# Kernel optimization log

Hardware: AMD Instinct MI355X
Metric: run time of the kernel (lower is better)

## Reference

```python
import jax, jax.numpy as jnp
import numpy as np

B, H, W, C, WS, NH, NL, ND = 64, 32, 32, 96, 8, 6, 4, 6
N = WS * WS
HD = C // NH
SC = HD ** -0.5


def _rel_pos_index():
    coords = np.stack(np.meshgrid(np.arange(WS), np.arange(WS), indexing='ij')).reshape(2, -1)
    rel = (coords[:, :, None] - coords[:, None, :]).transpose(1, 2, 0)
    rel[..., 0] += WS - 1
    rel[..., 1] += WS - 1
    rel[..., 0] *= 2 * WS - 1
    return jnp.asarray(rel.sum(-1))  # [N, N] int


def _attn_mask():
    shift = WS // 2
    img = np.zeros((H, W))
    cnt = 0
    for hs in (slice(0, -WS), slice(-WS, -shift), slice(-shift, None)):
        for ws_ in (slice(0, -WS), slice(-WS, -shift), slice(-shift, None)):
            img[hs, ws_] = cnt
            cnt += 1
    mw = img.reshape(H // WS, WS, W // WS, WS).transpose(0, 2, 1, 3).reshape(-1, N)
    am = mw[:, None, :] - mw[:, :, None]
    return jnp.asarray(np.where(am != 0, -100.0, 0.0).astype(np.float32))  # [nW, N, N]


RPI = _rel_pos_index()
AMASK = _attn_mask()


def ln(x, s, b):
    m = x.mean(-1, keepdims=True)
    v = ((x - m) ** 2).mean(-1, keepdims=True)
    return (x - m) * jax.lax.rsqrt(v + 1e-5) * s + b


def conv3(x, w, b):
    return jax.lax.conv_general_dilated(x, w, (1, 1), 'SAME', dimension_numbers=('NHWC', 'HWIO', 'NHWC')) + b


def win_part(x):  # (B,H,W,C) -> (B*nW, N, C)
    b = x.shape[0]
    return x.reshape(b, H // WS, WS, W // WS, WS, C).transpose(0, 1, 3, 2, 4, 5).reshape(-1, N, C)


def win_rev(xw, b):  # (B*nW, N, C) -> (B,H,W,C)
    return xw.reshape(b, H // WS, W // WS, WS, WS, C).transpose(0, 1, 3, 2, 4, 5).reshape(b, H, W, C)


def swin_block(x, shift, p):
    n1s, n1b, qw, qb, pw, pb, rpb, n2s, n2b, f1w, f1b, f2w, f2b = p
    b = x.shape[0]
    h = ln(x, n1s, n1b).reshape(b, H, W, C)
    if shift:
        h = jnp.roll(h, (-shift, -shift), (1, 2))
    xw = win_part(h)
    qkv = (xw @ qw + qb).reshape(-1, N, 3, NH, HD).transpose(2, 0, 3, 1, 4)
    q, k, v = qkv[0], qkv[1], qkv[2]  # each (B*nW, NH, N, HD)
    attn = (q * SC) @ k.transpose(0, 1, 3, 2)  # (B*nW, NH, N, N)
    bias = rpb[RPI.reshape(-1)].reshape(N, N, NH).transpose(2, 0, 1)
    attn = attn + bias[None]
    if shift:
        nW = AMASK.shape[0]
        attn = (attn.reshape(b, nW, NH, N, N) + AMASK[None, :, None]).reshape(-1, NH, N, N)
    attn = jax.nn.softmax(attn, -1)
    o = (attn @ v).transpose(0, 2, 1, 3).reshape(-1, N, C) @ pw + pb
    h = win_rev(o, b)
    if shift:
        h = jnp.roll(h, (shift, shift), (1, 2))
    x = x + h.reshape(b, H * W, C)
    y = ln(x, n2s, n2b)
    return x + jax.nn.gelu(y @ f1w + f1b, approximate=False) @ f2w + f2b


def setup_inputs() -> dict:
    key = jax.random.key(0)
    ks = iter(jax.random.split(key, 40))
    nrm = lambda shape: jax.random.normal(next(ks), shape, jnp.float32) * 0.02
    d = {
        'es_input': jax.random.normal(next(ks), (B, 2, H, W), jnp.float32),
        'j_plus_input': jax.random.normal(next(ks), (B, 2, H, W), jnp.float32),
        'conv_first_w': nrm((3, 3, 4, C)), 'conv_first_b': jnp.zeros((C,), jnp.float32),
        'pe_norm_s': jnp.ones((C,), jnp.float32), 'pe_norm_b': jnp.zeros((C,), jnp.float32),
        'n1_s': jnp.ones((NL, ND, C), jnp.float32), 'n1_b': jnp.zeros((NL, ND, C), jnp.float32),
        'qkv_w': nrm((NL, ND, C, 3 * C)), 'qkv_b': jnp.zeros((NL, ND, 3 * C), jnp.float32),
        'proj_w': nrm((NL, ND, C, C)), 'proj_b': jnp.zeros((NL, ND, C), jnp.float32),
        'rpb': nrm((NL, ND, (2 * WS - 1) ** 2, NH)),
        'n2_s': jnp.ones((NL, ND, C), jnp.float32), 'n2_b': jnp.zeros((NL, ND, C), jnp.float32),
        'fc1_w': nrm((NL, ND, C, 4 * C)), 'fc1_b': jnp.zeros((NL, ND, 4 * C), jnp.float32),
        'fc2_w': nrm((NL, ND, 4 * C, C)), 'fc2_b': jnp.zeros((NL, ND, C), jnp.float32),
        'rstb_conv_w': nrm((NL, 3, 3, C, C)), 'rstb_conv_b': jnp.zeros((NL, C), jnp.float32),
        'normf_s': jnp.ones((C,), jnp.float32), 'normf_b': jnp.zeros((C,), jnp.float32),
        'body_w': nrm((3, 3, C, C)), 'body_b': jnp.zeros((C,), jnp.float32),
        'last_w': nrm((3, 3, C, 2)), 'last_b': jnp.zeros((2,), jnp.float32),
    }
    return d


def reference(es_input, j_plus_input, conv_first_w, conv_first_b, pe_norm_s, pe_norm_b,
              n1_s, n1_b, qkv_w, qkv_b, proj_w, proj_b, rpb, n2_s, n2_b,
              fc1_w, fc1_b, fc2_w, fc2_b, rstb_conv_w, rstb_conv_b,
              normf_s, normf_b, body_w, body_b, last_w, last_b):
    x0 = jnp.concatenate([es_input, j_plus_input], 1).transpose(0, 2, 3, 1)  # NHWC, C=4
    xf = conv3(x0, conv_first_w, conv_first_b)  # shallow feature, [B,H,W,96]
    x = ln(xf.reshape(B, H * W, C), pe_norm_s, pe_norm_b)  # patch_embed norm
    for l in range(NL):
        r = x
        for d in range(ND):
            p = (n1_s[l, d], n1_b[l, d], qkv_w[l, d], qkv_b[l, d], proj_w[l, d], proj_b[l, d],
                 rpb[l, d], n2_s[l, d], n2_b[l, d], fc1_w[l, d], fc1_b[l, d], fc2_w[l, d], fc2_b[l, d])
            x = swin_block(x, 0 if d % 2 == 0 else WS // 2, p)
        x = conv3(x.reshape(B, H, W, C), rstb_conv_w[l], rstb_conv_b[l]).reshape(B, H * W, C) + r
    x = ln(x, normf_s, normf_b).reshape(B, H, W, C)
    res = conv3(x, body_w, body_b) + xf
    out = conv3(res, last_w, last_b)  # [B,H,W,2]
    return out.transpose(0, 3, 1, 2)
```

## Files before the change

kernel.cpp:

```cpp
#include <hip/hip_runtime.h>
#include <hip/hip_bf16.h>
#include <cstddef>
#include <cstdint>

#define BB 64
#define HH 32
#define WW_ 32
#define CC 96
#define WS 8
#define NH 6
#define NL 4
#define ND 6
#define T_TOK (BB*HH*WW_)
#define TC ((size_t)T_TOK*CC)

typedef long long ll;
typedef __attribute__((ext_vector_type(8))) short short8;
typedef __attribute__((ext_vector_type(4))) float f32x4;
typedef __attribute__((ext_vector_type(4))) unsigned short ushort4v;

__global__ void JNetSwinIR_41034117546277_kernel() {}

__device__ __forceinline__ unsigned short f2bf(float f) {
  unsigned u = __float_as_uint(f);
  unsigned r = (u + 0x7FFF + ((u >> 16) & 1)) >> 16;
  return (unsigned short)r;
}
__device__ __forceinline__ float bf2f(unsigned short h) {
  return __uint_as_float(((unsigned)h) << 16);
}

__global__ __launch_bounds__(256) void fill_kernel(float* p, float v, int n)
{
  const int idx = blockIdx.x * 256 + threadIdx.x;
  if (idx < n) p[idx] = v;
}

__global__ __launch_bounds__(256) void wconv_kernel(
    const float* __restrict__ W, unsigned short* __restrict__ Wt, int K, int N)
{
  const int ld = blockIdx.y;
  const int idx = blockIdx.x * 256 + threadIdx.x;
  if (idx >= K * N) return;
  const int k = idx / N, n = idx % N;
  Wt[(size_t)ld * K * N + (size_t)n * K + k] = f2bf(W[(size_t)ld * K * N + idx]);
}

__global__ __launch_bounds__(256) void wconv_conv_kernel(
    const float* __restrict__ W, unsigned short* __restrict__ Wt, int total)
{
  const int idx = blockIdx.x * 256 + threadIdx.x;
  if (idx >= total) return;
  const int l9 = idx / 9216;
  const int rest = idx % 9216;
  const int oc = rest / 96, ic = rest % 96;
  Wt[idx] = f2bf(W[(size_t)(l9 * 96 + ic) * 96 + oc]);
}

__global__ __launch_bounds__(256) void ln_fp32_kernel(
    const float* __restrict__ x, const float* __restrict__ gamma,
    const float* __restrict__ beta, float* __restrict__ out)
{
  const int wave = threadIdx.x >> 6;
  const int lane = threadIdx.x & 63;
  const int t = blockIdx.x * 4 + wave;
  const float* xp = x + (size_t)t * CC;
  const float v0 = xp[lane];
  const float v1 = (lane < 32) ? xp[64 + lane] : 0.f;
  float s = v0 + v1, s2 = v0 * v0 + v1 * v1;
  #pragma unroll
  for (int off = 32; off; off >>= 1) {
    s  += __shfl_xor(s,  off);
    s2 += __shfl_xor(s2, off);
  }
  const float mean = s * (1.f / 96.f);
  const float var  = s2 * (1.f / 96.f) - mean * mean;
  const float inv  = rsqrtf(var + 1e-5f);
  float* op = out + (size_t)t * CC;
  const float r0 = (v0 - mean) * inv * gamma[lane] + beta[lane];
  const float r1 = (v1 - mean) * inv * gamma[64 + lane] + beta[64 + lane];
  op[lane] = r0;
  if (lane < 32) op[64 + lane] = r1;
}

__global__ __launch_bounds__(384) void swin_block_fused(
    float* x, const float* __restrict__ n1s, const float* __restrict__ n1b,
    const unsigned short* __restrict__ wq_ld, const float* __restrict__ qkvb,
    const float* __restrict__ rpb_ld,
    const unsigned short* __restrict__ wp_ld, const float* __restrict__ projb,
    const float* __restrict__ n2s, const float* __restrict__ n2b,
    const unsigned short* __restrict__ w1_ld, const float* __restrict__ f1b,
    const unsigned short* __restrict__ w2_ld, const float* __restrict__ f2b,
    int shift)
{
  const int widx = blockIdx.x;
  const int tid  = threadIdx.x;
  const int wv   = tid >> 6;
  const int lane = tid & 63;

  __shared__ __attribute__((aligned(16))) char smem[72472];
  auto a    = (unsigned short(*)[104])(smem);
  auto kk   = (float(*)[100])(smem + 13312);
  auto xacc = (float(*)[100])(smem + 13312);
  auto vv   = (unsigned short(*)[104])(smem + 38912);
  auto hbuf = (unsigned short(*)[200])(smem + 38912);
  auto qt   = (unsigned short(*)[112])(smem + 52224);
  float* bias_s = (float*)(smem + 66560);
  int*   reg_s  = (int*)(smem + 71960);
  int*   st_s   = (int*)(smem + 72216);

  if (tid < 64) {
    const int wimg = widx & 15;
    const int h = (wimg >> 2) * 8 + (tid >> 3);
    const int w = (wimg & 3) * 8 + (tid & 7);
    reg_s[tid] = 3 * (h < 24 ? 0 : (h < 28 ? 1 : 2)) +
                     (w < 24 ? 0 : (w < 28 ? 1 : 2));
    const int b = widx >> 4;
    const int p = (h + shift) & 31, q = (w + shift) & 31;
    st_s[tid] = (b << 10) + (p << 5) + q;
  }
  for (int i = tid; i < NH * 225; i += 384) {
    const int hh = i / 225, ii = i % 225;
    bias_s[i] = rpb_ld[ii * NH + hh];
  }
  __syncthreads();

  for (int t = wv; t < 64; t += 6) {
    const float* xp = x + (size_t)st_s[t] * CC;
    const float v0 = xp[lane];
    const float v1 = (lane < 32) ? xp[64 + lane] : 0.f;
    float s = v0 + v1, s2 = v0 * v0 + v1 * v1;
    #pragma unroll
    for (int off = 32; off; off >>= 1) {
      s  += __shfl_xor(s,  off);
      s2 += __shfl_xor(s2, off);
    }
    const float mean = s * (1.f / 96.f);
    const float var  = s2 * (1.f / 96.f) - mean * mean;
    const float inv  = rsqrtf(var + 1e-5f);
    a[t][lane] = f2bf((v0 - mean) * inv * n1s[lane] + n1b[lane]);
    if (lane < 32)
      a[t][64 + lane] = f2bf((v1 - mean) * inv * n1s[64 + lane] + n1b[64 + lane]);
  }
  __syncthreads();

  {
    const int row = lane & 15;
    const int ko  = (lane >> 4) * 8;
    const int cc  = lane & 15;
    const int cr0 = (lane >> 4) * 4;
    #pragma unroll
    for (int out3 = 0; out3 < 3; ++out3) {
      const int n0 = out3 * 96 + wv * 16;
      const unsigned short* bp = wq_ld + (size_t)(n0 + row) * 96 + ko;
      const float bz = qkvb[n0 + cc];
      #pragma unroll
      for (int rt = 0; rt < 4; ++rt) {
        f32x4 acc = {0.f, 0.f, 0.f, 0.f};
        const unsigned short* ap = &a[rt * 16 + row][ko];
        #pragma unroll
        for (int k0 = 0; k0 < 96; k0 += 32) {
          const short8 af = *(const short8*)(ap + k0);
          const short8 bf = *(const short8*)(bp + k0);
          acc = __builtin_amdgcn_mfma_f32_16x16x32_bf16(af, bf, acc, 0, 0, 0);
        }
        #pragma unroll
        for (int r = 0; r < 4; ++r) {
          const int tok = rt * 16 + cr0 + r;
          const float v = acc[r] + bz;
          if (out3 == 0)      qt[tok][wv * 16 + cc] = f2bf(v);
          else if (out3 == 1) kk[tok][wv * 16 + cc] = v;
          else                vv[tok][wv * 16 + cc] = f2bf(v);
        }
      }
    }
  }
  __syncthreads();

  const int head = wv;
  {
    float q[16];
    {
      const short8 q0 = *(const short8*)&qt[lane][head * 16];
      const short8 q1 = *(const short8*)&qt[lane][head * 16 + 8];
      #pragma unroll
      for (int i = 0; i < 8; ++i) {
        q[i]     = bf2f((unsigned short)q0[i]);
        q[8 + i] = bf2f((unsigned short)q1[i]);
      }
    }
    const float* bias_h = bias_s + head * 225;
    const int ih = lane >> 3, iw = lane & 7;
    const int myreg = reg_s[lane];
    float s[64];
    #pragma unroll
    for (int j = 0; j < 64; ++j) {
      const float4 k0 = *(const float4*)&kk[j][head * 16];
      const float4 k1 = *(const float4*)&kk[j][head * 16 + 4];
      const float4 k2 = *(const float4*)&kk[j][head * 16 + 8];
      const float4 k3 = *(const float4*)&kk[j][head * 16 + 12];
      float acc = 0.f;
      acc = fmaf(q[0],  k0.x, acc); acc = fmaf(q[1],  k0.y, acc);
      acc = fmaf(q[2],  k0.z, acc); acc = fmaf(q[3],  k0.w, acc);
      acc = fmaf(q[4],  k1.x, acc); acc = fmaf(q[5],  k1.y, acc);
      acc = fmaf(q[6],  k1.z, acc); acc = fmaf(q[7],  k1.w, acc);
      acc = fmaf(q[8],  k2.x, acc); acc = fmaf(q[9],  k2.y, acc);
      acc = fmaf(q[10], k2.z, acc); acc = fmaf(q[11], k2.w, acc);
      acc = fmaf(q[12], k3.x, acc); acc = fmaf(q[13], k3.y, acc);
      acc = fmaf(q[14], k3.z, acc); acc = fmaf(q[15], k3.w, acc);
      const int idx = (ih - (j >> 3) + 7) * 15 + (iw - (j & 7) + 7);
      acc = acc * 0.25f + bias_h[idx];
      if (shift && reg_s[j] != myreg) acc -= 100.f;
      s[j] = acc;
    }
    float m = s[0];
    #pragma unroll
    for (int j = 1; j < 64; ++j) m = fmaxf(m, s[j]);
    float sum = 0.f;
    #pragma unroll
    for (int j = 0; j < 64; ++j) { const float p = __expf(s[j] - m); s[j] = p; sum += p; }
    const float inv = 1.f / sum;
    float o[16] = {};
    #pragma unroll
    for (int j = 0; j < 64; ++j) {
      const float p = s[j] * inv;
      const short8 v0 = *(const short8*)&vv[j][head * 16];
      const short8 v1 = *(const short8*)&vv[j][head * 16 + 8];
      #pragma unroll
      for (int i = 0; i < 8; ++i) {
        o[i]     = fmaf(p, bf2f((unsigned short)v0[i]), o[i]);
        o[8 + i] = fmaf(p, bf2f((unsigned short)v1[i]), o[8 + i]);
      }
    }
    short8 o0, o1;
    #pragma unroll
    for (int i = 0; i < 8; ++i) {
      o0[i] = (short)f2bf(o[i]);
      o1[i] = (short)f2bf(o[8 + i]);
    }
    *(short8*)&a[lane][head * 16]     = o0;
    *(short8*)&a[lane][head * 16 + 8] = o1;
  }
  __syncthreads();

  {
    const int row = lane & 15;
    const int ko  = (lane >> 4) * 8;
    const int cc  = lane & 15;
    const int cr0 = (lane >> 4) * 4;
    const int n0 = wv * 16;
    const unsigned short* bp = wp_ld + (size_t)(n0 + row) * 96 + ko;
    const float bz = projb[n0 + cc];
    #pragma unroll
    for (int rt = 0; rt < 4; ++rt) {
      f32x4 acc = {0.f, 0.f, 0.f, 0.f};
      const unsigned short* ap = &a[rt * 16 + row][ko];
      #pragma unroll
      for (int k0 = 0; k0 < 96; k0 += 32) {
        const short8 af = *(const short8*)(ap + k0);
        const short8 bf = *(const short8*)(bp + k0);
        acc = __builtin_amdgcn_mfma_f32_16x16x32_bf16(af, bf, acc, 0, 0, 0);
      }
      #pragma unroll
      for (int r = 0; r < 4; ++r) {
        const int tok = rt * 16 + cr0 + r;
        const float xo = x[(size_t)st_s[tok] * CC + n0 + cc];
        xacc[tok][n0 + cc] = xo + acc[r] + bz;
      }
    }
  }
  __syncthreads();

  for (int t = wv; t < 64; t += 6) {
    const float v0 = xacc[t][lane];
    const float v1 = (lane < 32) ? xacc[t][64 + lane] : 0.f;
    float s = v0 + v1, s2 = v0 * v0 + v1 * v1;
    #pragma unroll
    for (int off = 32; off; off >>= 1) {
      s  += __shfl_xor(s,  off);
      s2 += __shfl_xor(s2, off);
    }
    const float mean = s * (1.f / 96.f);
    const float var  = s2 * (1.f / 96.f) - mean * mean;
    const float inv  = rsqrtf(var + 1e-5f);
    a[t][lane] = f2bf((v0 - mean) * inv * n2s[lane] + n2b[lane]);
    if (lane < 32)
      a[t][64 + lane] = f2bf((v1 - mean) * inv * n2s[64 + lane] + n2b[64 + lane]);
  }
  __syncthreads();

  const int row = lane & 15;
  const int ko  = (lane >> 4) * 8;
  const int cc  = lane & 15;
  const int cr0 = (lane >> 4) * 4;
  f32x4 acc2[4];
  #pragma unroll
  for (int i = 0; i < 4; ++i) acc2[i] = (f32x4){0.f, 0.f, 0.f, 0.f};
  #pragma unroll
  for (int p = 0; p < 2; ++p) {
    #pragma unroll
    for (int ct = 0; ct < 2; ++ct) {
      const int n0g = p * 192 + wv * 32 + ct * 16;
      const int n0l = wv * 32 + ct * 16;
      const unsigned short* bp = w1_ld + (size_t)(n0g + row) * 96 + ko;
      const float bz = f1b[n0g + cc];
      #pragma unroll
      for (int rt = 0; rt < 4; ++rt) {
        f32x4 acc = {0.f, 0.f, 0.f, 0.f};
        const unsigned short* ap = &a[rt * 16 + row][ko];
        #pragma unroll
        for (int k0 = 0; k0 < 96; k0 += 32) {
          const short8 af = *(const short8*)(ap + k0);
          const short8 bf = *(const short8*)(bp + k0);
          acc = __builtin_amdgcn_mfma_f32_16x16x32_bf16(af, bf, acc, 0, 0, 0);
        }
        #pragma unroll
        for (int r = 0; r < 4; ++r) {
          float v = acc[r] + bz;
          v = 0.5f * v * (1.f + erff(v * 0.70710678118f));
          hbuf[rt * 16 + cr0 + r][n0l + cc] = f2bf(v);
        }
      }
    }
    __syncthreads();
    {
      const int n0 = wv * 16;
      const unsigned short* bp = w2_ld + (size_t)(n0 + row) * 384 + p * 192 + ko;
      #pragma unroll
      for (int rt = 0; rt < 4; ++rt) {
        const unsigned short* ap = &hbuf[rt * 16 + row][ko];
        #pragma unroll
        for (int k0 = 0; k0 < 192; k0 += 32) {
          const short8 af = *(const short8*)(ap + k0);
          const short8 bf = *(const short8*)(bp + k0);
          acc2[rt] = __builtin_amdgcn_mfma_f32_16x16x32_bf16(af, bf, acc2[rt], 0, 0, 0);
        }
      }
    }
    __syncthreads();
  }

  {
    const int n0 = wv * 16;
    const float bz = f2b[n0 + cc];
    #pragma unroll
    for (int rt = 0; rt < 4; ++rt) {
      #pragma unroll
      for (int r = 0; r < 4; ++r) {
        const int tok = rt * 16 + cr0 + r;
        x[(size_t)st_s[tok] * CC + n0 + cc] = xacc[tok][n0 + cc] + acc2[rt][r] + bz;
      }
    }
  }
}

__global__ __launch_bounds__(256) void copy_kernel(
    float* __restrict__ dst, const float* __restrict__ src)
{
  const int idx = blockIdx.x * 256 + threadIdx.x;
  dst[idx] = src[idx];
}

__global__ __launch_bounds__(256) void conv96m_kernel(
    const float* __restrict__ x, const unsigned short* __restrict__ wt,
    const float* __restrict__ bias, const float* resid, float* out)
{
  const int blk = blockIdx.x;
  const int b = blk >> 4, th = (blk >> 2) & 3, tw = blk & 3;
  const int h0 = th * 8, w0 = tw * 8;
  __shared__ unsigned short patch[100][104];
  for (int idx = threadIdx.x; idx < 100 * 24; idx += 256) {
    const int pp = idx / 24, c4 = (idx % 24) * 4;
    const int ph = pp / 10, pw = pp % 10;
    const int hh = h0 + ph - 1, ww = w0 + pw - 1;
    float4 v = {0.f, 0.f, 0.f, 0.f};
    if ((unsigned)hh < 32u && (unsigned)ww < 32u)
      v = *(const float4*)&x[(((size_t)b * 32 + hh) * 32 + ww) * 96 + c4];
    ushort4v o;
    o.x = f2bf(v.x); o.y = f2bf(v.y); o.z = f2bf(v.z); o.w = f2bf(v.w);
    *(ushort4v*)&patch[pp][c4] = o;
  }
  __syncthreads();
  const int wv = threadIdx.x >> 6, lane = threadIdx.x & 63;
  const int m0 = wv * 16;
  const int arow = lane & 15;
  const int ko  = (lane >> 4) * 8;
  const int px = m0 + arow;
  const int ph_ = px >> 3, pw_ = px & 7;
  f32x4 acc[6];
  #pragma unroll
  for (int i = 0; i < 6; ++i) acc[i] = (f32x4){0.f, 0.f, 0.f, 0.f};
  #pragma unroll
  for (int kh = 0; kh < 3; ++kh)
    #pragma unroll
    for (int kw = 0; kw < 3; ++kw) {
      const unsigned short* wbase = wt + (size_t)(kh * 3 + kw) * 9216;
      const unsigned short* prow = &patch[(ph_ + kh) * 10 + (pw_ + kw)][ko];
      #pragma unroll
      for (int k0 = 0; k0 < 96; k0 += 32) {
        const short8 af = *(const short8*)(prow + k0);
        #pragma unroll
        for (int nt = 0; nt < 6; ++nt) {
          const short8 bf = *(const short8*)(wbase + (size_t)(nt * 16 + arow) * 96 + ko + k0);
          acc[nt] = __builtin_amdgcn_mfma_f32_16x16x32_bf16(af, bf, acc[nt], 0, 0, 0);
        }
      }
    }
  const int cc = lane & 15;
  const int cr0 = (lane >> 4) * 4;
  #pragma unroll
  for (int nt = 0; nt < 6; ++nt) {
    const int oc = nt * 16 + cc;
    const float bz = bias[oc];
    #pragma unroll
    for (int r = 0; r < 4; ++r) {
      const int p = m0 + cr0 + r;
      const int h = p >> 3, w = p & 7;
      const size_t t = (((size_t)b * 32 + h0 + h) * 32 + (w0 + w));
      float v = acc[nt][r] + bz;
      if (resid) v += resid[t * 96 + oc];
      out[t * 96 + oc] = v;
    }
  }
}

__global__ __launch_bounds__(256) void conv_first_kernel(
    const float* __restrict__ es, const float* __restrict__ jp,
    const float* __restrict__ wgt, const float* __restrict__ bias,
    float* __restrict__ xf)
{
  const int idx = blockIdx.x * 256 + threadIdx.x;
  const int oc = idx % 96;
  const int pos = idx / 96;
  const int w = pos % 32, hp = (pos / 32) % 32, b = pos / 1024;
  float acc = bias[oc];
  for (int kh = 0; kh < 3; ++kh) {
    const int hh = hp + kh - 1;
    if ((unsigned)hh >= 32u) continue;
    for (int kw = 0; kw < 3; ++kw) {
      const int ww = w + kw - 1;
      if ((unsigned)ww >= 32u) continue;
      const size_t sp = ((size_t)b * 2 * 32 + hh) * 32 + ww;
      const float i0 = es[sp];
      const float i1 = es[sp + 1024];
      const float i2 = jp[sp];
      const float i3 = jp[sp + 1024];
      const float* wr = wgt + (size_t)((kh * 3 + kw) * 4) * 96 + oc;
      acc = fmaf(i0, wr[0], acc);
      acc = fmaf(i1, wr[96], acc);
      acc = fmaf(i2, wr[192], acc);
      acc = fmaf(i3, wr[288], acc);
    }
  }
  xf[idx] = acc;
}

__global__ __launch_bounds__(256) void conv_last_kernel(
    const float* __restrict__ res, const float* __restrict__ wgt,
    const float* __restrict__ bias, float* __restrict__ out)
{
  const int idx = blockIdx.x * 256 + threadIdx.x;
  const int oc = idx % 2;
  const int pos = idx / 2;
  const int w = pos % 32, hp = (pos / 32) % 32, b = pos / 1024;
  float acc = bias[oc];
  for (int kh = 0; kh < 3; ++kh) {
    const int hh = hp + kh - 1;
    if ((unsigned)hh >= 32u) continue;
    for (int kw = 0; kw < 3; ++kw) {
      const int ww = w + kw - 1;
      if ((unsigned)ww >= 32u) continue;
      const float* pr = res + (((size_t)b * 32 + hh) * 32 + ww) * 96;
      const float* wr = wgt + (size_t)((kh * 3 + kw) * 96) * 2 + oc;
      #pragma unroll 8
      for (int ic = 0; ic < 96; ++ic)
        acc = fmaf(pr[ic], wr[ic * 2], acc);
    }
  }
  out[(((size_t)b * 2 + oc) * 32 + hp) * 32 + w] = acc;
}

extern "C" void kernel_launch(void* const* d_in, const int* in_sizes, int n_in,
                              void* d_out, int out_size, void* d_ws, size_t ws_size,
                              hipStream_t stream)
{
  const int fill_grid = (out_size + 255) / 256;

  if (n_in != 27) {
    fill_kernel<<<fill_grid, 256, 0, stream>>>((float*)d_out, 200.0f + (float)n_in, out_size);
    return;
  }
  static const int expected_sizes[27] = {
    131072, 131072, 3456, 96, 96, 96, 2304, 2304, 663552, 6912,
    221184, 2304, 32400, 2304, 2304, 884736, 9216, 884736, 2304,
    331776, 384, 96, 96, 82944, 96, 1728, 2
  };
  for (int i = 0; i < 27; ++i) {
    if (in_sizes[i] != expected_sizes[i]) {
      fill_kernel<<<fill_grid, 256, 0, stream>>>((float*)d_out, 300.0f + (float)i, out_size);
      return;
    }
  }
  if (out_size != 131072) {
    fill_kernel<<<fill_grid, 256, 0, stream>>>((float*)d_out, 400.0f, out_size);
    return;
  }
  const uintptr_t raw = (uintptr_t)d_ws;
  const uintptr_t alignedp = (raw + 255) & ~(uintptr_t)255;
  const size_t ws_avail_bytes = (ws_size > (alignedp - raw)) ? ws_size - (alignedp - raw) : 0;
  const size_t avail = ws_avail_bytes / 4;
  const size_t WBUF_F = 1534464;
  const size_t floor_need = 2 * TC + WBUF_F;
  if (avail < floor_need) {
    fill_kernel<<<fill_grid, 256, 0, stream>>>((float*)d_out,
        100.0f + (float)(ws_size >> 20), out_size);
    return;
  }

  const float* es      = (const float*)d_in[0];
  const float* jp      = (const float*)d_in[1];
  const float* cf_w    = (const float*)d_in[2];
  const float* cf_b    = (const float*)d_in[3];
  const float* pe_s    = (const float*)d_in[4];
  const float* pe_b    = (const float*)d_in[5];
  const float* n1_s    = (const float*)d_in[6];
  const float* n1_b    = (const float*)d_in[7];
  const float* qkv_w   = (const float*)d_in[8];
  const float* qkv_b   = (const float*)d_in[9];
  const float* proj_w  = (const float*)d_in[10];
  const float* proj_b  = (const float*)d_in[11];
  const float* rpb     = (const float*)d_in[12];
  const float* n2_s    = (const float*)d_in[13];
  const float* n2_b    = (const float*)d_in[14];
  const float* fc1_w   = (const float*)d_in[15];
  const float* fc1_b   = (const float*)d_in[16];
  const float* fc2_w   = (const float*)d_in[17];
  const float* fc2_b   = (const float*)d_in[18];
  const float* rstb_w  = (const float*)d_in[19];
  const float* rstb_b  = (const float*)d_in[20];
  const float* nf_s    = (const float*)d_in[21];
  const float* nf_b    = (const float*)d_in[22];
  const float* body_w  = (const float*)d_in[23];
  const float* body_b  = (const float*)d_in[24];
  const float* last_w  = (const float*)d_in[25];
  const float* last_b  = (const float*)d_in[26];

  float* x = (float*)alignedp;
  float* r = x + TC;
  unsigned short* wq  = (unsigned short*)(r + TC);
  unsigned short* wp  = wq + 663552;
  unsigned short* w1  = wp + 221184;
  unsigned short* w2  = w1 + 884736;
  unsigned short* wcr = w2 + 884736;
  unsigned short* wcb = wcr + 331776;

  const int grid_tc = (int)(TC / 256);
  const int grid_lf = T_TOK / 4;
  const int nwin = T_TOK / 64;

  wconv_kernel<<<dim3((96 * 288 + 255) / 256, 24), 256, 0, stream>>>(qkv_w, wq, 96, 288);
  wconv_kernel<<<dim3((96 * 96 + 255) / 256, 24), 256, 0, stream>>>(proj_w, wp, 96, 96);
  wconv_kernel<<<dim3((96 * 384 + 255) / 256, 24), 256, 0, stream>>>(fc1_w, w1, 96, 384);
  wconv_kernel<<<dim3((384 * 96 + 255) / 256, 24), 256, 0, stream>>>(fc2_w, w2, 384, 96);
  wconv_conv_kernel<<<(331776 + 255) / 256, 256, 0, stream>>>(rstb_w, wcr, 331776);
  wconv_conv_kernel<<<(82944 + 255) / 256, 256, 0, stream>>>(body_w, wcb, 82944);

  conv_first_kernel<<<grid_tc, 256, 0, stream>>>(es, jp, cf_w, cf_b, x);
  ln_fp32_kernel<<<grid_lf, 256, 0, stream>>>(x, pe_s, pe_b, x);

  float* xb = x;
  float* rb = r;
  for (int l = 0; l < NL; ++l) {
    copy_kernel<<<grid_tc, 256, 0, stream>>>(rb, xb);
    for (int d = 0; d < ND; ++d) {
      const int ld = l * ND + d;
      const int shift = (d & 1) ? 4 : 0;
      swin_block_fused<<<nwin, 384, 0, stream>>>(
          xb, n1_s + ld * CC, n1_b + ld * CC,
          wq + (size_t)ld * 288 * 96, qkv_b + (size_t)ld * 288,
          rpb + (size_t)ld * 225 * NH,
          wp + (size_t)ld * 96 * 96, proj_b + (size_t)ld * 96,
          n2_s + ld * CC, n2_b + ld * CC,
          w1 + (size_t)ld * 384 * 96, fc1_b + (size_t)ld * 384,
          w2 + (size_t)ld * 96 * 384, fc2_b + (size_t)ld * 96, shift);
    }
    conv96m_kernel<<<1024, 256, 0, stream>>>(xb, wcr + (size_t)l * 9 * 9216,
                                             rstb_b + (size_t)l * CC, rb, rb);
    float* sw = xb; xb = rb; rb = sw;
  }
  ln_fp32_kernel<<<grid_lf, 256, 0, stream>>>(xb, nf_s, nf_b, rb);
  conv_first_kernel<<<grid_tc, 256, 0, stream>>>(es, jp, cf_w, cf_b, xb);
  conv96m_kernel<<<1024, 256, 0, stream>>>(rb, wcb, body_b, xb, xb);
  conv_last_kernel<<<(BB * 32 * 32 * 2) / 256, 256, 0, stream>>>(xb, last_w, last_b, (float*)d_out);
}
```

Measured before the change: 4.114 ms.

## Use MFMA for window attention and drop residual copy via triple buffering

Replaces the per-lane scalar QK^T and PV loops in the fused Swin block with bf16 MFMA tiles. Softmax is done in registers with cross-lane shuffles, probabilities are staged as bf16 in shared memory and V is stored transposed. K is now stored as bf16 instead of fp32, which lowers accuracy slightly and changes the shared-memory layout. Separately, when the workspace is large enough, a third activation buffer lets the LN and conv kernels write the residual copy directly, removing the per-layer copy kernel.

Result: faster. 3.890 ms (-5.5%).

```diff
diff --git a/kernel.cpp b/kernel.cpp
--- a/kernel.cpp
+++ b/kernel.cpp
@@ -59,7 +59,7 @@
 
 __global__ __launch_bounds__(256) void ln_fp32_kernel(
     const float* __restrict__ x, const float* __restrict__ gamma,
-    const float* __restrict__ beta, float* __restrict__ out)
+    const float* __restrict__ beta, float* __restrict__ out, float* out2)
 {
   const int wave = threadIdx.x >> 6;
   const int lane = threadIdx.x & 63;
@@ -76,11 +76,14 @@
   const float mean = s * (1.f / 96.f);
   const float var  = s2 * (1.f / 96.f) - mean * mean;
   const float inv  = rsqrtf(var + 1e-5f);
-  float* op = out + (size_t)t * CC;
   const float r0 = (v0 - mean) * inv * gamma[lane] + beta[lane];
   const float r1 = (v1 - mean) * inv * gamma[64 + lane] + beta[64 + lane];
-  op[lane] = r0;
-  if (lane < 32) op[64 + lane] = r1;
+  out[(size_t)t * CC + lane] = r0;
+  if (lane < 32) out[(size_t)t * CC + 64 + lane] = r1;
+  if (out2) {
+    out2[(size_t)t * CC + lane] = r0;
+    if (lane < 32) out2[(size_t)t * CC + 64 + lane] = r1;
+  }
 }
 
 __global__ __launch_bounds__(384) void swin_block_fused(
@@ -98,16 +101,17 @@
   const int wv   = tid >> 6;
   const int lane = tid & 63;
 
-  __shared__ __attribute__((aligned(16))) char smem[72472];
+  __shared__ __attribute__((aligned(16))) char smem[73496];
   auto a    = (unsigned short(*)[104])(smem);
-  auto kk   = (float(*)[100])(smem + 13312);
+  auto kk   = (unsigned short(*)[104])(smem + 13312);
   auto xacc = (float(*)[100])(smem + 13312);
-  auto vv   = (unsigned short(*)[104])(smem + 38912);
-  auto hbuf = (unsigned short(*)[200])(smem + 38912);
-  auto qt   = (unsigned short(*)[112])(smem + 52224);
-  float* bias_s = (float*)(smem + 66560);
-  int*   reg_s  = (int*)(smem + 71960);
-  int*   st_s   = (int*)(smem + 72216);
+  unsigned short* vvT = (unsigned short*)(smem + 26624);
+  auto qt   = (unsigned short(*)[104])(smem + 40448);
+  auto hbuf = (unsigned short(*)[200])(smem + 40448);
+  unsigned short* pbuf = (unsigned short*)(smem + 53760);
+  float* bias_s = (float*)(smem + 67584);
+  int*   reg_s  = (int*)(smem + 72984);
+  int*   st_s   = (int*)(smem + 73240);
 
   if (tid < 64) {
     const int wimg = widx & 15;
@@ -169,77 +173,87 @@
           const int tok = rt * 16 + cr0 + r;
           const float v = acc[r] + bz;
           if (out3 == 0)      qt[tok][wv * 16 + cc] = f2bf(v);
-          else if (out3 == 1) kk[tok][wv * 16 + cc] = v;
-          else                vv[tok][wv * 16 + cc] = f2bf(v);
+          else if (out3 == 1) kk[tok][wv * 16 + cc] = f2bf(v);
+          else                vvT[(wv * 16 + cc) * 72 + tok] = f2bf(v);
         }
       }
     }
   }
   __syncthreads();
 
-  const int head = wv;
   {
-    float q[16];
+    const int head = wv;
+    const int g  = lane >> 4;
+    const int cc = lane & 15;
+    const bool lo = (lane < 32);
+    const float* bias_h = bias_s + head * 225;
+    unsigned short* pb = pbuf + head * (16 * 72);
+    const short8 z8 = {0, 0, 0, 0, 0, 0, 0, 0};
+    short8 vf0, vf1;
     {
-      const short8 q0 = *(const short8*)&qt[lane][head * 16];
-      const short8 q1 = *(const short8*)&qt[lane][head * 16 + 8];
-      #pragma unroll
-      for (int i = 0; i < 8; ++i) {
-        q[i]     = bf2f((unsigned short)q0[i]);
-        q[8 + i] = bf2f((unsigned short)q1[i]);
-      }
-    }
-    const float* bias_h = bias_s + head * 225;
-    const int ih = lane >> 3, iw = lane & 7;
-    const int myreg = reg_s[lane];
-    float s[64];
-    #pragma unroll
-    for (int j = 0; j < 64; ++j) {
-      const float4 k0 = *(const float4*)&kk[j][head * 16];
-      const float4 k1 = *(const float4*)&kk[j][head * 16 + 4];
-      const float4 k2 = *(const float4*)&kk[j][head * 16 + 8];
-      const float4 k3 = *(const float4*)&kk[j][head * 16 + 12];
-      float acc = 0.f;
-      acc = fmaf(q[0],  k0.x, acc); acc = fmaf(q[1],  k0.y, acc);
-      acc = fmaf(q[2],  k0.z, acc); acc = fmaf(q[3],  k0.w, acc);
-      acc = fmaf(q[4],  k1.x, acc); acc = fmaf(q[5],  k1.y, acc);
-      acc = fmaf(q[6],  k1.z, acc); acc = fmaf(q[7],  k1.w, acc);
-      acc = fmaf(q[8],  k2.x, acc); acc = fmaf(q[9],  k2.y, acc);
-      acc = fmaf(q[10], k2.z, acc); acc = fmaf(q[11], k2.w, acc);
-      acc = fmaf(q[12], k3.x, acc); acc = fmaf(q[13], k3.y, acc);
-      acc = fmaf(q[14], k3.z, acc); acc = fmaf(q[15], k3.w, acc);
-      const int idx = (ih - (j >> 3) + 7) * 15 + (iw - (j & 7) + 7);
-      acc = acc * 0.25f + bias_h[idx];
-      if (shift && reg_s[j] != myreg) acc -= 100.f;
-      s[j] = acc;
-    }
-    float m = s[0];
-    #pragma unroll
-    for (int j = 1; j < 64; ++j) m = fmaxf(m, s[j]);
-    float sum = 0.f;
-    #pragma unroll
-    for (int j = 0; j < 64; ++j) { const float p = __expf(s[j] - m); s[j] = p; sum += p; }
-    const float inv = 1.f / sum;
-    float o[16] = {};
-    #pragma unroll
-    for (int j = 0; j < 64; ++j) {
-      const float p = s[j] * inv;
-      const short8 v0 = *(const short8*)&vv[j][head * 16];
-      const short8 v1 = *(const short8*)&vv[j][head * 16 + 8];
-      #pragma unroll
-      for (int i = 0; i < 8; ++i) {
-        o[i]     = fmaf(p, bf2f((unsigned short)v0[i]), o[i]);
-        o[8 + i] = fmaf(p, bf2f((unsigned short)v1[i]), o[8 + i]);
-      }
-    }
-    short8 o0, o1;
-    #pragma unroll
-    for (int i = 0; i < 8; ++i) {
-      o0[i] = (short)f2bf(o[i]);
-      o1[i] = (short)f2bf(o[8 + i]);
-    }
-    *(short8*)&a[lane][head * 16]     = o0;
-    *(short8*)&a[lane][head * 16 + 8] = o1;
+      const unsigned short* vp = vvT + (size_t)(head * 16 + cc) * 72 + g * 8;
+      vf0 = *(const short8*)(vp);
+      vf1 = *(const short8*)(vp + 32);
+    }
+    #pragma unroll
+    for (int qtile = 0; qtile < 4; ++qtile) {
+      short8 af = z8;
+      if (lo) af = *(const short8*)&qt[qtile * 16 + cc][head * 16 + g * 8];
+      f32x4 sa[4];
+      #pragma unroll
+      for (int kt = 0; kt < 4; ++kt) {
+        short8 bf = z8;
+        if (lo) bf = *(const short8*)&kk[kt * 16 + cc][head * 16 + g * 8];
+        const f32x4 zero = {0.f, 0.f, 0.f, 0.f};
+        sa[kt] = __builtin_amdgcn_mfma_f32_16x16x32_bf16(af, bf, zero, 0, 0, 0);
+      }
+      float p[4][4];
+      #pragma unroll
+      for (int r = 0; r < 4; ++r) {
+        const int i = qtile * 16 + g * 4 + r;
+        const int ih = i >> 3, iw = i & 7;
+        const int ri = reg_s[i];
+        float mx = -1e30f;
+        #pragma unroll
+        for (int kt = 0; kt < 4; ++kt) {
+          const int j = kt * 16 + cc;
+          const int idx = (ih - (j >> 3) + 7) * 15 + (iw - (j & 7) + 7);
+          float v = sa[kt][r] * 0.25f + bias_h[idx];
+          if (shift && reg_s[j] != ri) v -= 100.f;
+          p[kt][r] = v;
+          mx = fmaxf(mx, v);
+        }
+        mx = fmaxf(mx, __shfl_xor(mx, 1));
+        mx = fmaxf(mx, __shfl_xor(mx, 2));
+        mx = fmaxf(mx, __shfl_xor(mx, 4));
+        mx = fmaxf(mx, __shfl_xor(mx, 8));
+        float sum = 0.f;
+        #pragma unroll
+        for (int kt = 0; kt < 4; ++kt) {
+          p[kt][r] = __expf(p[kt][r] - mx);
+          sum += p[kt][r];
+        }
+        sum += __shfl_xor(sum, 1);
+        sum += __shfl_xor(sum, 2);
+        sum += __shfl_xor(sum, 4);
+        sum += __shfl_xor(sum, 8);
+        const float is = 1.f / sum;
+        #pragma unroll
+        for (int kt = 0; kt < 4; ++kt)
+          pb[(g * 4 + r) * 72 + kt * 16 + cc] = f2bf(p[kt][r] * is);
+      }
+      f32x4 oa = {0.f, 0.f, 0.f, 0.f};
+      {
+        const unsigned short* pp = pb + cc * 72 + g * 8;
+        const short8 pf0 = *(const short8*)(pp);
+        const short8 pf1 = *(const short8*)(pp + 32);
+        oa = __builtin_amdgcn_mfma_f32_16x16x32_bf16(pf0, vf0, oa, 0, 0, 0);
+        oa = __builtin_amdgcn_mfma_f32_16x16x32_bf16(pf1, vf1, oa, 0, 0, 0);
+      }
+      #pragma unroll
+      for (int r = 0; r < 4; ++r)
+        a[qtile * 16 + g * 4 + r][head * 16 + cc] = f2bf(oa[r]);
+    }
   }
   __syncthreads();
 
@@ -363,7 +377,7 @@
 
 __global__ __launch_bounds__(256) void conv96m_kernel(
     const float* __restrict__ x, const unsigned short* __restrict__ wt,
-    const float* __restrict__ bias, const float* resid, float* out)
+    const float* __restrict__ bias, const float* resid, float* out, float* out2)
 {
   const int blk = blockIdx.x;
   const int b = blk >> 4, th = (blk >> 2) & 3, tw = blk & 3;
@@ -420,6 +434,7 @@
       float v = acc[nt][r] + bz;
       if (resid) v += resid[t * 96 + oc];
       out[t * 96 + oc] = v;
+      if (out2) out2[t * 96 + oc] = v;
     }
   }
 }
@@ -510,12 +525,12 @@
   const size_t ws_avail_bytes = (ws_size > (alignedp - raw)) ? ws_size - (alignedp - raw) : 0;
   const size_t avail = ws_avail_bytes / 4;
   const size_t WBUF_F = 1534464;
-  const size_t floor_need = 2 * TC + WBUF_F;
-  if (avail < floor_need) {
+  if (avail < 2 * TC + WBUF_F) {
     fill_kernel<<<fill_grid, 256, 0, stream>>>((float*)d_out,
         100.0f + (float)(ws_size >> 20), out_size);
     return;
   }
+  const bool rot = (avail >= 3 * TC + WBUF_F);
 
   const float* es      = (const float*)d_in[0];
   const float* jp      = (const float*)d_in[1];
@@ -545,11 +560,13 @@
   const float* last_w  = (const float*)d_in[25];
   const float* last_b  = (const float*)d_in[26];
 
-  float* x = (float*)alignedp;
-  float* r = x + TC;
-  unsigned short* wq  = (unsigned short*)(r + TC);
-  unsigned short* wp  = wq + 663552;
-  unsigned short* w1  = wp + 221184;
+  float* base = (float*)alignedp;
+  float* x  = base;
+  float* r  = base + TC;
+  float* sp = rot ? base + 2 * TC : nullptr;
+  unsigned short* wq  = (unsigned short*)(base + (rot ? 3 : 2) * TC);
+  unsigned short* wpj = wq + 663552;
+  unsigned short* w1  = wpj + 221184;
   unsigned short* w2  = w1 + 884736;
   unsigned short* wcr = w2 + 884736;
   unsigned short* wcb = wcr + 331776;
@@ -559,19 +576,20 @@
   const int nwin = T_TOK / 64;
 
   wconv_kernel<<<dim3((96 * 288 + 255) / 256, 24), 256, 0, stream>>>(qkv_w, wq, 96, 288);
-  wconv_kernel<<<dim3((96 * 96 + 255) / 256, 24), 256, 0, stream>>>(proj_w, wp, 96, 96);
+  wconv_kernel<<<dim3((96 * 96 + 255) / 256, 24), 256, 0, stream>>>(proj_w, wpj, 96, 96);
   wconv_kernel<<<dim3((96 * 384 + 255) / 256, 24), 256, 0, stream>>>(fc1_w, w1, 96, 384);
   wconv_kernel<<<dim3((384 * 96 + 255) / 256, 24), 256, 0, stream>>>(fc2_w, w2, 384, 96);
   wconv_conv_kernel<<<(331776 + 255) / 256, 256, 0, stream>>>(rstb_w, wcr, 331776);
   wconv_conv_kernel<<<(82944 + 255) / 256, 256, 0, stream>>>(body_w, wcb, 82944);
 
   conv_first_kernel<<<grid_tc, 256, 0, stream>>>(es, jp, cf_w, cf_b, x);
-  ln_fp32_kernel<<<grid_lf, 256, 0, stream>>>(x, pe_s, pe_b, x);
+  ln_fp32_kernel<<<grid_lf, 256, 0, stream>>>(x, pe_s, pe_b, x, rot ? r : nullptr);
 
   float* xb = x;
   float* rb = r;
+  float* sb = sp;
   for (int l = 0; l < NL; ++l) {
-    copy_kernel<<<grid_tc, 256, 0, stream>>>(rb, xb);
+    if (!rot) copy_kernel<<<grid_tc, 256, 0, stream>>>(rb, xb);
     for (int d = 0; d < ND; ++d) {
       const int ld = l * ND + d;
       const int shift = (d & 1) ? 4 : 0;
@@ -579,17 +597,23 @@
           xb, n1_s + ld * CC, n1_b + ld * CC,
           wq + (size_t)ld * 288 * 96, qkv_b + (size_t)ld * 288,
           rpb + (size_t)ld * 225 * NH,
-          wp + (size_t)ld * 96 * 96, proj_b + (size_t)ld * 96,
+          wpj + (size_t)ld * 96 * 96, proj_b + (size_t)ld * 96,
           n2_s + ld * CC, n2_b + ld * CC,
           w1 + (size_t)ld * 384 * 96, fc1_b + (size_t)ld * 384,
           w2 + (size_t)ld * 96 * 384, fc2_b + (size_t)ld * 96, shift);
     }
-    conv96m_kernel<<<1024, 256, 0, stream>>>(xb, wcr + (size_t)l * 9 * 9216,
-                                             rstb_b + (size_t)l * CC, rb, rb);
-    float* sw = xb; xb = rb; rb = sw;
-  }
-  ln_fp32_kernel<<<grid_lf, 256, 0, stream>>>(xb, nf_s, nf_b, rb);
+    if (rot) {
+      conv96m_kernel<<<1024, 256, 0, stream>>>(xb, wcr + (size_t)l * 9 * 9216,
+                                               rstb_b + (size_t)l * CC, rb, rb, sb);
+      float* t = xb; xb = sb; sb = t;
+    } else {
+      conv96m_kernel<<<1024, 256, 0, stream>>>(xb, wcr + (size_t)l * 9 * 9216,
+                                               rstb_b + (size_t)l * CC, rb, rb, nullptr);
+      float* t = xb; xb = rb; rb = t;
+    }
+  }
+  ln_fp32_kernel<<<grid_lf, 256, 0, stream>>>(xb, nf_s, nf_b, rb, nullptr);
   conv_first_kernel<<<grid_tc, 256, 0, stream>>>(es, jp, cf_w, cf_b, xb);
-  conv96m_kernel<<<1024, 256, 0, stream>>>(rb, wcb, body_b, xb, xb);
+  conv96m_kernel<<<1024, 256, 0, stream>>>(rb, wcb, body_b, xb, xb, nullptr);
   conv_last_kernel<<<(BB * 32 * 32 * 2) / 256, 256, 0, stream>>>(xb, last_w, last_b, (float*)d_out);
 }
```
